# Optimization experiments

Measured on AMD Instinct MI355X. Metric: run time of the kernel, lower is better.

The kernel has to match this reference:

```python
import math
import jax, jax.numpy as jnp
import numpy as np

B, S, D = 4, 2048, 1024
L = 2                      # codec_decoder_transformer_lengths entry
H, HD = 8, 128             # n_heads == n_kv_heads (no GQA repeat)
FF = 4096
WINDOW = 16                # sliding window (causal: keys in [i-16, i])
NORM_EPS = 0.01
QK_EPS = 1e-6
SCALE_INIT = 0.1           # layer_id < 18 -> 0.1


def _alibi_slopes(n):
    # n is a power of 2 here (8)
    r = 2.0 ** (-8.0 / n)
    return jnp.array([r ** (i + 1) for i in range(n)], dtype=jnp.float32)


def rms_norm(x, w, eps):
    return x * jax.lax.rsqrt(jnp.mean(x * x, axis=-1, keepdims=True) + eps) * w


def _attn_bias(dtype):
    pos = jnp.arange(S)
    rel = pos[None, :] - pos[:, None]          # [S,S], rel = j - i
    slopes = _alibi_slopes(H).astype(dtype)
    bias = slopes[:, None, None] * rel[None].astype(dtype)   # [H,S,S]
    mask = (rel > 0) | (rel < -WINDOW)         # causal + sliding window
    return jnp.where(mask[None], -jnp.inf, bias)


def setup_inputs() -> dict:
    key = jax.random.key(0)
    ks = jax.random.split(key, 9)
    sd = 0.02
    w = lambda k, shape: jax.random.normal(k, shape, jnp.float32) * sd
    return {
        "x": jax.random.normal(ks[0], (B, S, D), jnp.float32),
        "wq": w(ks[1], (L, D, H * HD)),
        "wk": w(ks[2], (L, D, H * HD)),
        "wv": w(ks[3], (L, D, H * HD)),
        "wo": w(ks[4], (L, H * HD, D)),
        "q_norm_w": jnp.ones((L, H * HD), jnp.float32),
        "k_norm_w": jnp.ones((L, H * HD), jnp.float32),
        "w1": w(ks[5], (L, D, FF)),
        "w2": w(ks[6], (L, FF, D)),
        "w3": w(ks[7], (L, D, FF)),
        "attn_norm_w": jnp.ones((L, D), jnp.float32),
        "ffn_norm_w": jnp.ones((L, D), jnp.float32),
        "attn_scale": jnp.full((L, D), SCALE_INIT, jnp.float32),
        "ffn_scale": jnp.full((L, D), SCALE_INIT, jnp.float32),
    }


def reference(x, wq, wk, wv, wo, q_norm_w, k_norm_w, w1, w2, w3,
              attn_norm_w, ffn_norm_w, attn_scale, ffn_scale):
    bias = _attn_bias(x.dtype)                 # [H,S,S]
    inv_sqrt_d = 1.0 / math.sqrt(HD)

    def block(h, p):
        (lwq, lwk, lwv, lwo, qnw, knw, lw1, lw2, lw3, anw, fnw, asc, fsc) = p
        xn = rms_norm(h, anw, NORM_EPS)
        # qk_norm applied on the flat (H*HD) projection before the head split
        q = rms_norm(xn @ lwq, qnw, QK_EPS).reshape(B, S, H, HD).transpose(0, 2, 1, 3)
        k = rms_norm(xn @ lwk, knw, QK_EPS).reshape(B, S, H, HD).transpose(0, 2, 1, 3)
        v = (xn @ lwv).reshape(B, S, H, HD).transpose(0, 2, 1, 3)
        scores = jnp.einsum('bhqd,bhkd->bhqk', q, k) * inv_sqrt_d + bias[None]
        attn = jax.nn.softmax(scores, axis=-1)
        y = jnp.einsum('bhqk,bhkd->bhqd', attn, v)
        y = y.transpose(0, 2, 1, 3).reshape(B, S, H * HD)
        h = h + asc * (y @ lwo)
        xn = rms_norm(h, fnw, NORM_EPS)
        ff = (jax.nn.silu(xn @ lw1) * (xn @ lw3)) @ lw2
        return h + fsc * ff, None

    out, _ = jax.lax.scan(
        block, x,
        (wq, wk, wv, wo, q_norm_w, k_norm_w, w1, w2, w3,
         attn_norm_w, ffn_norm_w, attn_scale, ffn_scale))
    return out
```

## Files before the change

kernel.cpp:

```cpp
#include <hip/hip_runtime.h>

#define B_ 4
#define S_ 2048
#define D_ 1024
#define H_ 8
#define HD_ 128
#define FF_ 4096
#define R_ (B_*S_)

typedef __attribute__((ext_vector_type(8))) short short8;
typedef __attribute__((ext_vector_type(4))) float f32x4;

__device__ __forceinline__ unsigned short f2bf(float f) {
  unsigned int u = __float_as_uint(f);
  return (unsigned short)((u + 0x7fffu + ((u >> 16) & 1u)) >> 16);
}
__device__ __forceinline__ float bf2f(unsigned short s) {
  return __uint_as_float(((unsigned int)s) << 16);
}

typedef const __attribute__((address_space(1))) unsigned int* gas_p;
typedef __attribute__((address_space(3))) unsigned int* las_p;
__device__ __forceinline__ void gload16(const void* g, void* l) {
  __builtin_amdgcn_global_load_lds((gas_p)g, (las_p)l, 16, 0, 0);
}

__global__ __launch_bounds__(256) void f2bf_t_all(
    const float* __restrict__ wq, const float* __restrict__ wk,
    const float* __restrict__ wv, const float* __restrict__ wo,
    const float* __restrict__ w1, const float* __restrict__ w3,
    const float* __restrict__ w2,
    unsigned short* __restrict__ qkvt, unsigned short* __restrict__ wot,
    unsigned short* __restrict__ w1t, unsigned short* __restrict__ w3t,
    unsigned short* __restrict__ w2t) {
  const int id = blockIdx.x;
  const int l = id >> 14, r = id & 16383;
  const float* src; unsigned short* dst; int Rows, Cols, t2;
  if (r < 4096) {
    Rows = 1024; Cols = 1024; t2 = r & 1023;
    const int wsel = r >> 10;
    if (wsel == 0)      { src = wq + (size_t)l*1048576u; dst = qkvt + (size_t)l*3145728u; }
    else if (wsel == 1) { src = wk + (size_t)l*1048576u; dst = qkvt + (size_t)l*3145728u + 1048576u; }
    else if (wsel == 2) { src = wv + (size_t)l*1048576u; dst = qkvt + (size_t)l*3145728u + 2097152u; }
    else                { src = wo + (size_t)l*1048576u; dst = wot + (size_t)l*1048576u; }
  } else if (r < 12288) {
    Rows = 1024; Cols = 4096; t2 = (r - 4096) & 4095;
    if (r < 8192) { src = w1 + (size_t)l*4194304u; dst = w1t + (size_t)l*4194304u; }
    else          { src = w3 + (size_t)l*4194304u; dst = w3t + (size_t)l*4194304u; }
  } else {
    Rows = 4096; Cols = 1024; t2 = r - 12288;
    src = w2 + (size_t)l*4194304u; dst = w2t + (size_t)l*4194304u;
  }
  const int lgc = (Cols == 4096) ? 7 : 5;
  const int bx = t2 & ((1 << lgc) - 1), by = t2 >> lgc;
  const int r0 = by * 32, c0 = bx * 32;
  __shared__ float tile[32][33];
  const int tx = threadIdx.x & 31, ty = threadIdx.x >> 5;
  #pragma unroll
  for (int j = 0; j < 32; j += 8)
    tile[ty + j][tx] = src[(size_t)(r0 + ty + j) * Cols + c0 + tx];
  __syncthreads();
  #pragma unroll
  for (int j = 0; j < 32; j += 8)
    dst[(size_t)(c0 + ty + j) * Rows + r0 + tx] = f2bf(tile[tx][ty + j]);
}

__global__ __launch_bounds__(256) void rmsnorm_f2b(const float* __restrict__ in,
    const float* __restrict__ w, unsigned short* __restrict__ out, float eps) {
  const int row = blockIdx.x, t = threadIdx.x;
  const float4 xv = *(const float4*)&in[(size_t)row * D_ + t * 4];
  float p = xv.x*xv.x + xv.y*xv.y + xv.z*xv.z + xv.w*xv.w;
  #pragma unroll
  for (int off = 32; off >= 1; off >>= 1) p += __shfl_xor(p, off);
  __shared__ float red[4];
  if ((t & 63) == 0) red[t >> 6] = p;
  __syncthreads();
  float scl = rsqrtf((red[0] + red[1] + red[2] + red[3]) * (1.0f / D_) + eps);
  const float4 wv = *(const float4*)&w[t * 4];
  ((ushort4*)out)[(size_t)row * 256 + t] = make_ushort4(
      f2bf(xv.x*scl*wv.x), f2bf(xv.y*scl*wv.y), f2bf(xv.z*scl*wv.z), f2bf(xv.w*scl*wv.w));
}

__global__ __launch_bounds__(256) void qknorm_k(unsigned short* __restrict__ qkv,
    const float* __restrict__ qw, const float* __restrict__ kw) {
  const int row = blockIdx.x, t = threadIdx.x;
  unsigned short* qp = qkv + (size_t)row * 3072;
  unsigned short* kp = qp + 1024;
  const ushort4 qv = ((const ushort4*)qp)[t];
  const ushort4 kv = ((const ushort4*)kp)[t];
  float q0 = bf2f(qv.x), q1 = bf2f(qv.y), q2 = bf2f(qv.z), q3 = bf2f(qv.w);
  float k0 = bf2f(kv.x), k1 = bf2f(kv.y), k2 = bf2f(kv.z), k3 = bf2f(kv.w);
  float pq = q0*q0 + q1*q1 + q2*q2 + q3*q3;
  float pk = k0*k0 + k1*k1 + k2*k2 + k3*k3;
  #pragma unroll
  for (int off = 32; off >= 1; off >>= 1) { pq += __shfl_xor(pq, off); pk += __shfl_xor(pk, off); }
  __shared__ float redq[4], redk[4];
  if ((t & 63) == 0) { redq[t >> 6] = pq; redk[t >> 6] = pk; }
  __syncthreads();
  float sq = rsqrtf((redq[0]+redq[1]+redq[2]+redq[3]) * (1.0f / D_) + 1e-6f);
  float sk = rsqrtf((redk[0]+redk[1]+redk[2]+redk[3]) * (1.0f / D_) + 1e-6f);
  const float4 qwv = *(const float4*)&qw[t * 4];
  const float4 kwv = *(const float4*)&kw[t * 4];
  ((ushort4*)qp)[t] = make_ushort4(f2bf(q0*sq*qwv.x), f2bf(q1*sq*qwv.y),
                                   f2bf(q2*sq*qwv.z), f2bf(q3*sq*qwv.w));
  ((ushort4*)kp)[t] = make_ushort4(f2bf(k0*sk*kwv.x), f2bf(k1*sk*kwv.y),
                                   f2bf(k2*sk*kwv.z), f2bf(k3*sk*kwv.w));
}

__global__ __launch_bounds__(256) void attn_k(const unsigned short* __restrict__ qkv,
    unsigned short* __restrict__ y) {
  const int lane = threadIdx.x & 63;
  const int wid = (blockIdx.x * 256 + threadIdx.x) >> 6;
  const int qq = lane >> 4, li = lane & 15;
  const int grp = wid & (S_/4 - 1);
  const int bh  = wid >> 9;
  const int hh = bh & (H_ - 1);
  const int b  = bh >> 3;
  const int i  = grp * 4 + qq;
  const float slope = exp2f(-(float)(hh + 1));
  const float inv = 0.088388347648318447f;
  const size_t rowq = ((size_t)(b * S_ + i)) * 3072 + hh * HD_ + li * 8;
  const short8 qv8 = *(const short8*)&qkv[rowq];
  float qf[8];
  #pragma unroll
  for (int e = 0; e < 8; ++e) qf[e] = bf2f((unsigned short)qv8[e]);
  float sc[17];
  #pragma unroll
  for (int jj = 0; jj < 17; ++jj) {
    int j = i - 16 + jj;
    int jc = j < 0 ? 0 : j;
    size_t koff = ((size_t)(b * S_ + jc)) * 3072 + 1024 + hh * HD_ + li * 8;
    short8 kv = *(const short8*)&qkv[koff];
    float p = 0.f;
    #pragma unroll
    for (int e = 0; e < 8; ++e) p += qf[e] * bf2f((unsigned short)kv[e]);
    p += __shfl_xor(p, 8); p += __shfl_xor(p, 4);
    p += __shfl_xor(p, 2); p += __shfl_xor(p, 1);
    sc[jj] = (j >= 0) ? (p * inv + slope * (float)(jj - 16)) : -1e30f;
  }
  float m = sc[0];
  #pragma unroll
  for (int jj = 1; jj < 17; ++jj) m = fmaxf(m, sc[jj]);
  float wsum = 0.f, ax[8];
  #pragma unroll
  for (int e = 0; e < 8; ++e) ax[e] = 0.f;
  #pragma unroll
  for (int jj = 0; jj < 17; ++jj) {
    int j = i - 16 + jj;
    int jc = j < 0 ? 0 : j;
    float wgt = expf(sc[jj] - m);
    size_t voff = ((size_t)(b * S_ + jc)) * 3072 + 2048 + hh * HD_ + li * 8;
    short8 vv = *(const short8*)&qkv[voff];
    wsum += wgt;
    #pragma unroll
    for (int e = 0; e < 8; ++e) ax[e] += wgt * bf2f((unsigned short)vv[e]);
  }
  float rs = 1.f / wsum;
  short8 ov;
  #pragma unroll
  for (int e = 0; e < 8; ++e) ov[e] = (short)f2bf(ax[e] * rs);
  size_t yoff = ((size_t)(b * S_ + i)) * 1024 + hh * HD_ + li * 8;
  *(short8*)&y[yoff] = ov;
}

__device__ __forceinline__ void stage_tile(const unsigned short* __restrict__ src,
    unsigned short* lds, int rowbase, int K, int k0, int t) {
  #pragma unroll
  for (int it = 0; it < 4; ++it) {
    int g = it * 256 + t;
    int row = g >> 3, slot = g & 7;
    int sc8 = (slot ^ (row & 7)) << 3;
    gload16(&src[(size_t)(rowbase + row) * K + k0 + sc8], &lds[g * 8]);
  }
}

template<int EPI>
__global__ __launch_bounds__(256, 2) void gemm_tn(
    const unsigned short* __restrict__ A, const unsigned short* __restrict__ Bt,
    void* __restrict__ Cout, const float* __restrict__ sc,
    const float* __restrict__ x2, int M, int N, int K) {
  __shared__ __align__(16) unsigned short As[128 * 64];
  __shared__ __align__(16) unsigned short Bs[128 * 64];
  const int t = threadIdx.x;
  const int lane = t & 63, w = t >> 6;
  const int wr = w >> 1, wc = w & 1;
  const int br = blockIdx.y * 128, bc = blockIdx.x * 128;
  const int lr = lane & 15, lk = lane >> 4;
  const int xm = lr & 7;
  f32x4 acc[4][4];
  #pragma unroll
  for (int mi = 0; mi < 4; ++mi)
    #pragma unroll
    for (int ni = 0; ni < 4; ++ni) { f32x4 z = {0.f,0.f,0.f,0.f}; acc[mi][ni] = z; }
  for (int k0 = 0; k0 < K; k0 += 64) {
    stage_tile(A,  As, br, K, k0, t);
    stage_tile(Bt, Bs, bc, K, k0, t);
    __syncthreads();
    #pragma unroll
    for (int kk = 0; kk < 2; ++kk) {
      short8 af[4], bfr[4];
      #pragma unroll
      for (int mi = 0; mi < 4; ++mi)
        af[mi] = *(const short8*)&As[(wr*64 + mi*16 + lr) * 64 + (((kk*4 + lk) ^ xm) << 3)];
      #pragma unroll
      for (int ni = 0; ni < 4; ++ni)
        bfr[ni] = *(const short8*)&Bs[(wc*64 + ni*16 + lr) * 64 + (((kk*4 + lk) ^ xm) << 3)];
      #pragma unroll
      for (int mi = 0; mi < 4; ++mi)
        #pragma unroll
        for (int ni = 0; ni < 4; ++ni)
          acc[mi][ni] = __builtin_amdgcn_mfma_f32_16x16x32_bf16(af[mi], bfr[ni], acc[mi][ni], 0, 0, 0);
    }
    __syncthreads();
  }
  if (EPI == 0) {
    unsigned short* C = (unsigned short*)Cout;
    #pragma unroll
    for (int mi = 0; mi < 4; ++mi)
      #pragma unroll
      for (int ni = 0; ni < 4; ++ni) {
        int row = br + wr * 64 + mi * 16 + lk * 4;
        int col = bc + wc * 64 + ni * 16 + lr;
        #pragma unroll
        for (int r = 0; r < 4; ++r)
          C[(size_t)(row + r) * N + col] = f2bf(acc[mi][ni][r]);
      }
  } else if (EPI == 1) {
    float* hp = (float*)Cout;
    #pragma unroll
    for (int ni = 0; ni < 4; ++ni) {
      int col = bc + wc * 64 + ni * 16 + lr;
      float sv = sc[col];
      #pragma unroll
      for (int mi = 0; mi < 4; ++mi) {
        int row = br + wr * 64 + mi * 16 + lk * 4;
        #pragma unroll
        for (int r = 0; r < 4; ++r)
          hp[(size_t)(row + r) * N + col] += sv * acc[mi][ni][r];
      }
    }
  } else {
    float* hp = (float*)Cout;
    #pragma unroll
    for (int ni = 0; ni < 4; ++ni) {
      int col = bc + wc * 64 + ni * 16 + lr;
      float sv = sc[col];
      #pragma unroll
      for (int mi = 0; mi < 4; ++mi) {
        int row = br + wr * 64 + mi * 16 + lk * 4;
        #pragma unroll
        for (int r = 0; r < 4; ++r)
          hp[(size_t)(row + r) * N + col] = x2[(size_t)(row + r) * N + col] + sv * acc[mi][ni][r];
      }
    }
  }
}

__global__ __launch_bounds__(256, 2) void gemm_w13(
    const unsigned short* __restrict__ A, const unsigned short* __restrict__ B1t,
    const unsigned short* __restrict__ B3t, unsigned short* __restrict__ G,
    int M, int N, int K) {
  __shared__ __align__(16) unsigned short As[128 * 64];
  __shared__ __align__(16) unsigned short B1s[128 * 64];
  __shared__ __align__(16) unsigned short B3s[128 * 64];
  const int t = threadIdx.x;
  const int lane = t & 63, w = t >> 6;
  const int wr = w >> 1, wc = w & 1;
  const int br = blockIdx.y * 128, bc = blockIdx.x * 128;
  const int lr = lane & 15, lk = lane >> 4;
  const int xm = lr & 7;
  f32x4 acc1[4][4], acc3[4][4];
  #pragma unroll
  for (int mi = 0; mi < 4; ++mi)
    #pragma unroll
    for (int ni = 0; ni < 4; ++ni) {
      f32x4 z = {0.f,0.f,0.f,0.f}; acc1[mi][ni] = z; acc3[mi][ni] = z;
    }
  for (int k0 = 0; k0 < K; k0 += 64) {
    stage_tile(A,   As,  br, K, k0, t);
    stage_tile(B1t, B1s, bc, K, k0, t);
    stage_tile(B3t, B3s, bc, K, k0, t);
    __syncthreads();
    #pragma unroll
    for (int kk = 0; kk < 2; ++kk) {
      short8 af[4], b1r[4], b3r[4];
      #pragma unroll
      for (int mi = 0; mi < 4; ++mi)
        af[mi] = *(const short8*)&As[(wr*64 + mi*16 + lr) * 64 + (((kk*4 + lk) ^ xm) << 3)];
      #pragma unroll
      for (int ni = 0; ni < 4; ++ni) {
        b1r[ni] = *(const short8*)&B1s[(wc*64 + ni*16 + lr) * 64 + (((kk*4 + lk) ^ xm) << 3)];
        b3r[ni] = *(const short8*)&B3s[(wc*64 + ni*16 + lr) * 64 + (((kk*4 + lk) ^ xm) << 3)];
      }
      #pragma unroll
      for (int mi = 0; mi < 4; ++mi)
        #pragma unroll
        for (int ni = 0; ni < 4; ++ni) {
          acc1[mi][ni] = __builtin_amdgcn_mfma_f32_16x16x32_bf16(af[mi], b1r[ni], acc1[mi][ni], 0, 0, 0);
          acc3[mi][ni] = __builtin_amdgcn_mfma_f32_16x16x32_bf16(af[mi], b3r[ni], acc3[mi][ni], 0, 0, 0);
        }
    }
    __syncthreads();
  }
  #pragma unroll
  for (int mi = 0; mi < 4; ++mi)
    #pragma unroll
    for (int ni = 0; ni < 4; ++ni) {
      int row = br + wr * 64 + mi * 16 + lk * 4;
      int col = bc + wc * 64 + ni * 16 + lr;
      #pragma unroll
      for (int r = 0; r < 4; ++r) {
        float a1 = acc1[mi][ni][r], a3 = acc3[mi][ni][r];
        G[(size_t)(row + r) * N + col] = f2bf(a1 / (1.f + expf(-a1)) * a3);
      }
    }
}

extern "C" void kernel_launch(void* const* d_in, const int* in_sizes, int n_in,
                              void* d_out, int out_size, void* d_ws, size_t ws_size,
                              hipStream_t stream) {
  const float* x    = (const float*)d_in[0];
  const float* wq   = (const float*)d_in[1];
  const float* wk   = (const float*)d_in[2];
  const float* wv   = (const float*)d_in[3];
  const float* wo   = (const float*)d_in[4];
  const float* qnw  = (const float*)d_in[5];
  const float* knw  = (const float*)d_in[6];
  const float* w1   = (const float*)d_in[7];
  const float* w2   = (const float*)d_in[8];
  const float* w3   = (const float*)d_in[9];
  const float* anw  = (const float*)d_in[10];
  const float* fnw  = (const float*)d_in[11];
  const float* asc  = (const float*)d_in[12];
  const float* fsc  = (const float*)d_in[13];

  const size_t MB = 1024 * 1024;
  if (ws_size < 144 * MB) return;

  float* h = (float*)d_out;
  char* ws = (char*)d_ws;
  unsigned short* qkvt = (unsigned short*)ws;
  unsigned short* wot  = qkvt + 2u * 3145728u;
  unsigned short* w1t  = wot  + 2u * 1048576u;
  unsigned short* w3t  = w1t  + 2u * 4194304u;
  unsigned short* w2t  = w3t  + 2u * 4194304u;
  unsigned short* xn   = (unsigned short*)(ws + 64 * MB);
  unsigned short* qkv  = (unsigned short*)(ws + 80 * MB);
  unsigned short* gate = qkv;

  f2bf_t_all<<<32768, 256, 0, stream>>>(wq, wk, wv, wo, w1, w3, w2,
                                        qkvt, wot, w1t, w3t, w2t);

  for (int l = 0; l < 2; ++l) {
    rmsnorm_f2b<<<R_, 256, 0, stream>>>(l == 0 ? x : h, anw + l * D_, xn, 0.01f);
    gemm_tn<0><<<dim3(24, 64), 256, 0, stream>>>(xn, qkvt + (size_t)l*3145728u, qkv,
                                                 nullptr, nullptr, R_, 3072, 1024);
    qknorm_k<<<R_, 256, 0, stream>>>(qkv, qnw + l * 1024, knw + l * 1024);
    attn_k<<<R_ * H_ / 16, 256, 0, stream>>>(qkv, xn);
    if (l == 0)
      gemm_tn<2><<<dim3(8, 64), 256, 0, stream>>>(xn, wot, h, asc, x, R_, 1024, 1024);
    else
      gemm_tn<1><<<dim3(8, 64), 256, 0, stream>>>(xn, wot + 1048576u, h, asc + D_,
                                                  nullptr, R_, 1024, 1024);
    rmsnorm_f2b<<<R_, 256, 0, stream>>>(h, fnw + l * D_, xn, 0.01f);
    gemm_w13<<<dim3(32, 64), 256, 0, stream>>>(xn, w1t + (size_t)l*4194304u,
                                               w3t + (size_t)l*4194304u, gate, R_, 4096, 1024);
    gemm_tn<1><<<dim3(8, 64), 256, 0, stream>>>(gate, w2t + (size_t)l*4194304u, h,
                                                fsc + l * D_, nullptr, R_, 1024, 4096);
  }
}
```

Before: 853.5 us.

## Add triple-buffered 256x128 GEMM for N=1024 projections with residual epilogue

Introduces gemm_dp, a 512-thread kernel using 256x128 output tiles with a three-stage LDS ring fed by global_load_lds, register-prefetched fragments and raised wave priority around the MFMA block. It replaces gemm_tn for the output projection and the w2 down-projection, which have N=1024. The goal is to hide global-load latency and improve reuse per tile. The trade-off is fewer blocks (256) and one block per CU at 144KB of LDS, which may leave CUs underfilled on a 256-CU part.

```diff
diff --git a/kernel.cpp b/kernel.cpp
--- a/kernel.cpp
+++ b/kernel.cpp
@@ -256,6 +256,99 @@
   }
 }
 
+template<int EPI>
+__global__ __launch_bounds__(512, 1) void gemm_dp(
+    const unsigned short* __restrict__ A, const unsigned short* __restrict__ Bt,
+    float* __restrict__ hp, const float* __restrict__ sc,
+    const float* __restrict__ x2, int M, int N, int K) {
+  __shared__ __align__(16) unsigned short lds[3][24576];
+  const int t = threadIdx.x;
+  const int lane = t & 63, w = t >> 6;
+  const int wm = w >> 2, wn = w & 3;
+  const int lr = lane & 15, lk = lane >> 4;
+  const int xm = lr & 7;
+  const int br = blockIdx.y << 8, bc = blockIdx.x << 7;
+
+  const unsigned short* Ab = A + (size_t)br * K;
+  const unsigned short* Bb = Bt + (size_t)bc * K;
+
+  auto stage = [&](int buf, int k0) {
+    unsigned short* d = lds[buf];
+    #pragma unroll
+    for (int j = 0; j < 4; ++j) {
+      int idx = t + (j << 9);
+      int row = idx >> 3, slot = idx & 7;
+      gload16(Ab + (size_t)row * K + k0 + ((slot ^ (row & 7)) << 3),
+              &d[row * 64 + slot * 8]);
+    }
+    #pragma unroll
+    for (int j = 0; j < 2; ++j) {
+      int idx = t + (j << 9);
+      int row = idx >> 3, slot = idx & 7;
+      gload16(Bb + (size_t)row * K + k0 + ((slot ^ (row & 7)) << 3),
+              &d[16384 + row * 64 + slot * 8]);
+    }
+  };
+
+  f32x4 acc[8][2];
+  #pragma unroll
+  for (int mi = 0; mi < 8; ++mi)
+    #pragma unroll
+    for (int ni = 0; ni < 2; ++ni) { f32x4 z = {0.f,0.f,0.f,0.f}; acc[mi][ni] = z; }
+
+  const int NT = K >> 6;
+  stage(0, 0); stage(1, 64);
+  asm volatile("s_waitcnt vmcnt(6)" ::: "memory");
+  __builtin_amdgcn_s_barrier();
+
+  #pragma unroll 1
+  for (int kt = 0; kt < NT; ++kt) {
+    const unsigned short* cur = lds[kt % 3];
+    short8 af[2][8], bfr[2][2];
+    #pragma unroll
+    for (int ks = 0; ks < 2; ++ks) {
+      #pragma unroll
+      for (int mf = 0; mf < 8; ++mf)
+        af[ks][mf] = *(const short8*)&cur[(wm*128 + mf*16 + lr)*64 + (((ks*4+lk)^xm)<<3)];
+      #pragma unroll
+      for (int nf = 0; nf < 2; ++nf)
+        bfr[ks][nf] = *(const short8*)&cur[16384 + (wn*32 + nf*16 + lr)*64 + (((ks*4+lk)^xm)<<3)];
+    }
+    const int kp = (kt + 2 < NT) ? ((kt + 2) << 6) : 0;
+    stage((kt + 2) % 3, kp);
+    asm volatile("s_waitcnt vmcnt(6)" ::: "memory");
+    asm volatile("s_waitcnt lgkmcnt(0)" ::: "memory");
+    __builtin_amdgcn_sched_barrier(0);
+    __builtin_amdgcn_s_barrier();
+    __builtin_amdgcn_s_setprio(1);
+    #pragma unroll
+    for (int mf = 0; mf < 8; ++mf)
+      #pragma unroll
+      for (int nf = 0; nf < 2; ++nf)
+        #pragma unroll
+        for (int ks = 0; ks < 2; ++ks)
+          acc[mf][nf] = __builtin_amdgcn_mfma_f32_16x16x32_bf16(af[ks][mf], bfr[ks][nf], acc[mf][nf], 0, 0, 0);
+    __builtin_amdgcn_s_setprio(0);
+  }
+
+  #pragma unroll
+  for (int nf = 0; nf < 2; ++nf) {
+    int col = bc + wn*32 + nf*16 + lr;
+    float sv = sc[col];
+    #pragma unroll
+    for (int mf = 0; mf < 8; ++mf) {
+      int row = br + wm*128 + mf*16 + lk*4;
+      #pragma unroll
+      for (int r = 0; r < 4; ++r) {
+        if (EPI == 1)
+          hp[(size_t)(row + r) * N + col] += sv * acc[mf][nf][r];
+        else
+          hp[(size_t)(row + r) * N + col] = x2[(size_t)(row + r) * N + col] + sv * acc[mf][nf][r];
+      }
+    }
+  }
+}
+
 __global__ __launch_bounds__(256, 2) void gemm_w13(
     const unsigned short* __restrict__ A, const unsigned short* __restrict__ B1t,
     const unsigned short* __restrict__ B3t, unsigned short* __restrict__ G,
@@ -358,14 +451,14 @@
     qknorm_k<<<R_, 256, 0, stream>>>(qkv, qnw + l * 1024, knw + l * 1024);
     attn_k<<<R_ * H_ / 16, 256, 0, stream>>>(qkv, xn);
     if (l == 0)
-      gemm_tn<2><<<dim3(8, 64), 256, 0, stream>>>(xn, wot, h, asc, x, R_, 1024, 1024);
+      gemm_dp<2><<<dim3(8, 32), 512, 0, stream>>>(xn, wot, h, asc, x, R_, 1024, 1024);
     else
-      gemm_tn<1><<<dim3(8, 64), 256, 0, stream>>>(xn, wot + 1048576u, h, asc + D_,
+      gemm_dp<1><<<dim3(8, 32), 512, 0, stream>>>(xn, wot + 1048576u, h, asc + D_,
                                                   nullptr, R_, 1024, 1024);
     rmsnorm_f2b<<<R_, 256, 0, stream>>>(h, fnw + l * D_, xn, 0.01f);
     gemm_w13<<<dim3(32, 64), 256, 0, stream>>>(xn, w1t + (size_t)l*4194304u,
                                                w3t + (size_t)l*4194304u, gate, R_, 4096, 1024);
-    gemm_tn<1><<<dim3(8, 64), 256, 0, stream>>>(gate, w2t + (size_t)l*4194304u, h,
+    gemm_dp<1><<<dim3(8, 32), 512, 0, stream>>>(gate, w2t + (size_t)l*4194304u, h,
                                                 fsc + l * D_, nullptr, R_, 1024, 4096);
   }
 }
```

Measured after the change: 823.0 us (median of 3 runs). -3.6%, faster.
